# Kernel tuning notes

Hardware: AMD Instinct MI355X
Metric: run time of the kernel (lower is better)

Reference implementation:

```python
import jax, jax.numpy as jnp
import numpy as np

N, E, G = 100000, 1600000, 1024
BN_EPS = 1e-5
NEG_SLOPE = 0.2


def setup_inputs() -> dict:
    key = jax.random.key(0)
    ks = jax.random.split(key, 8)
    x = jax.random.normal(ks[0], (N, 128), dtype=jnp.float32)
    edge_index = jax.random.randint(ks[1], (2, E), 0, N, dtype=jnp.int64)
    batch = jnp.sort(jax.random.randint(ks[2], (N,), 0, G, dtype=jnp.int64))
    Wl = jax.random.normal(ks[3], (3, 128, 128), dtype=jnp.float32) * 0.08
    bl = jnp.zeros((3, 128), dtype=jnp.float32)
    Wr = jax.random.normal(ks[4], (3, 128, 128), dtype=jnp.float32) * 0.08
    bn_gamma = jnp.ones((3, 128), dtype=jnp.float32)
    bn_beta = jnp.zeros((3, 128), dtype=jnp.float32)
    bn2_gamma = jnp.ones((128,), dtype=jnp.float32)
    bn2_beta = jnp.zeros((128,), dtype=jnp.float32)
    fc_W = jax.random.normal(ks[5], (128, 64), dtype=jnp.float32) * 0.08
    fc_b = jnp.zeros((64,), dtype=jnp.float32)
    return {"x": x, "edge_index": edge_index, "batch": batch, "Wl": Wl, "bl": bl,
            "Wr": Wr, "bn_gamma": bn_gamma, "bn_beta": bn_beta,
            "bn2_gamma": bn2_gamma, "bn2_beta": bn2_beta, "fc_W": fc_W, "fc_b": fc_b}


def _batch_norm(h, gamma, beta):
    # training-mode BatchNorm1d: batch statistics, biased variance
    mu = jnp.mean(h, axis=0)
    var = jnp.mean((h - mu) ** 2, axis=0)
    return gamma * (h - mu) * jax.lax.rsqrt(var + BN_EPS) + beta


def reference(x, edge_index, batch, Wl, bl, Wr, bn_gamma, bn_beta,
              bn2_gamma, bn2_beta, fc_W, fc_b):
    src, dst = edge_index[0], edge_index[1]
    # in-degree of each destination node (for mean aggregation)
    deg = jax.ops.segment_sum(jnp.ones((E,), dtype=x.dtype), dst, num_segments=N)
    inv_deg = jnp.where(deg > 0, 1.0 / jnp.maximum(deg, 1.0), 0.0)[:, None]  # [N,1]
    h = x
    for i in range(3):
        # SAGEConv: out = lin_l(mean_{j in N(i)} h_j) + lin_r(h_i)
        agg = jax.ops.segment_sum(h[src], dst, num_segments=N) * inv_deg  # [N,H]
        h = agg @ Wl[i] + bl[i] + h @ Wr[i]
        h = jax.nn.leaky_relu(_batch_norm(h, bn_gamma[i], bn_beta[i]), NEG_SLOPE)
        # dropout omitted (eval-mode / deterministic reference)
    pooled = jax.ops.segment_sum(h, batch, num_segments=G)  # [G,H] global_add_pool
    out = _batch_norm(pooled, bn2_gamma, bn2_beta) @ fc_W + fc_b  # [G,latent]
    return out
```

## Files before the change

kernel.cpp:

```cpp
#include <hip/hip_runtime.h>

#define HD 128
#define NCOPY 32
#define BSH 8
#define BSZ 256
#define EPB 4096

typedef __attribute__((ext_vector_type(8))) short short8;
typedef __attribute__((ext_vector_type(4))) float f32x4;

union ABu { unsigned long long u[2]; short8 s8; };

__device__ inline float bf2f(ushort u) {
    union { unsigned int i; float f; } x; x.i = ((unsigned int)u) << 16; return x.f;
}
__device__ inline float bflo(unsigned int u) {
    union { unsigned int i; float f; } x; x.i = u << 16; return x.f;
}
__device__ inline float bfhi(unsigned int u) {
    union { unsigned int i; float f; } x; x.i = u & 0xffff0000u; return x.f;
}
__device__ inline ushort f2bf(float f) {
    union { float f; unsigned int i; } x; x.f = f;
    unsigned int r = x.i + 0x7FFF + ((x.i >> 16) & 1);
    return (ushort)(r >> 16);
}


__global__ __launch_bounds__(256) void kp_count(const int* __restrict__ dst,
                                                int* __restrict__ bucketCount, int E, int NB) {
    __shared__ int hist[512];
    for (int i = threadIdx.x; i < NB; i += 256) hist[i] = 0;
    __syncthreads();
    int e0 = blockIdx.x * EPB;
#pragma unroll
    for (int j = 0; j < 16; ++j) {
        int e = e0 + j * 256 + threadIdx.x;
        if (e < E) atomicAdd(&hist[dst[e] >> BSH], 1);
    }
    __syncthreads();
    for (int i = threadIdx.x; i < NB; i += 256)
        if (hist[i]) atomicAdd(&bucketCount[i], hist[i]);
}

__global__ void kp_scan(const int* __restrict__ bucketCount, int* __restrict__ bucketBase,
                        int* __restrict__ gCursor, int NB, int E) {
    __shared__ int lds[512];
    int tid = threadIdx.x;
    int v = (tid < NB) ? bucketCount[tid] : 0;
    lds[tid] = v;
    __syncthreads();
    for (int off = 1; off < 512; off <<= 1) {
        int t = 0;
        if (tid >= off) t = lds[tid - off];
        __syncthreads();
        if (tid >= off) lds[tid] += t;
        __syncthreads();
    }
    int excl = lds[tid] - v;
    if (tid < NB) { bucketBase[tid] = excl; gCursor[tid] = excl; }
    if (tid == 0) bucketBase[NB] = E;
}

__global__ __launch_bounds__(256) void kp_part(const int* __restrict__ src,
                                               const int* __restrict__ dst,
                                               int* __restrict__ gCursor,
                                               unsigned int* __restrict__ packed, int E, int NB) {
    __shared__ int hist[512], lbase[512], lcur[512];
    for (int i = threadIdx.x; i < NB; i += 256) hist[i] = 0;
    __syncthreads();
    int e0 = blockIdx.x * EPB;
    int b[16]; unsigned int w[16];
#pragma unroll
    for (int j = 0; j < 16; ++j) {
        int e = e0 + j * 256 + threadIdx.x;
        b[j] = -1;
        if (e < E) {
            int d = dst[e];
            int s = src[e];
            b[j] = d >> BSH;
            w[j] = (unsigned int)s | (((unsigned int)d & (BSZ - 1)) << 17);
            atomicAdd(&hist[b[j]], 1);
        }
    }
    __syncthreads();
    for (int i = threadIdx.x; i < NB; i += 256) {
        int c = hist[i];
        lbase[i] = c ? atomicAdd(&gCursor[i], c) : 0;
        lcur[i] = 0;
    }
    __syncthreads();
#pragma unroll
    for (int j = 0; j < 16; ++j) {
        if (b[j] >= 0) {
            int r = atomicAdd(&lcur[b[j]], 1);
            packed[lbase[b[j]] + r] = w[j];
        }
    }
}

__global__ __launch_bounds__(256) void kp_degfill(const unsigned int* __restrict__ packed,
                                                  const int* __restrict__ bucketBase,
                                                  int* __restrict__ rowptr,
                                                  float* __restrict__ inv,
                                                  int* __restrict__ csr, int N, int E) {
    __shared__ int dcnt[BSZ];
    __shared__ int scn[BSZ];
    __shared__ int rp[BSZ];
    int bkt = blockIdx.x;
    int tid = threadIdx.x;
    int n0 = bkt << BSH;
    dcnt[tid] = 0;
    __syncthreads();
    int beg = bucketBase[bkt], end = bucketBase[bkt + 1];
    for (int e = beg + tid; e < end; e += 256)
        atomicAdd(&dcnt[packed[e] >> 17], 1);
    __syncthreads();
    int v = dcnt[tid];
    scn[tid] = v;
    __syncthreads();
    for (int off = 1; off < 256; off <<= 1) {
        int t = 0;
        if (tid >= off) t = scn[tid - off];
        __syncthreads();
        if (tid >= off) scn[tid] += t;
        __syncthreads();
    }
    int rpv = beg + scn[tid] - v;
    int n = n0 + tid;
    if (n < N) {
        rowptr[n] = rpv;
        inv[n] = (v > 0) ? (1.0f / (float)v) : 0.0f;
    }
    if (bkt == 0 && tid == 0) rowptr[N] = E;
    __syncthreads();
    dcnt[tid] = 0;
    rp[tid] = rpv;
    __syncthreads();
    for (int e = beg + tid; e < end; e += 256) {
        unsigned int wv = packed[e];
        int ld = wv >> 17;
        int p = atomicAdd(&dcnt[ld], 1);
        csr[rp[ld] + p] = (int)(wv & 0x1FFFF);
    }
}

__global__ void k_prep(const float* __restrict__ x, ushort* __restrict__ xb, int total4,
                       const float* __restrict__ Wl, const float* __restrict__ Wr,
                       ushort* __restrict__ WT, int wtTotal) {
    int i = blockIdx.x * blockDim.x + threadIdx.x;
    int stride = gridDim.x * blockDim.x;
    for (int idx = i; idx < total4; idx += stride) {
        float4 v = ((const float4*)x)[idx];
        ushort4 o;
        o.x = f2bf(v.x); o.y = f2bf(v.y); o.z = f2bf(v.z); o.w = f2bf(v.w);
        ((ushort4*)xb)[idx] = o;
    }
    for (int idx = i; idx < wtTotal; idx += stride) {
        int l = idx >> 15;
        int rem = idx & 32767;
        int col = rem >> 8;
        int k = rem & 255;
        float v = (k < 128) ? Wl[l * 16384 + k * 128 + col]
                            : Wr[l * 16384 + (k - 128) * 128 + col];
        WT[idx] = f2bf(v);
    }
}

__global__ __launch_bounds__(256) void k_agg(const ushort* __restrict__ h,
                                             const int* __restrict__ rowptr,
                                             const int* __restrict__ csr,
                                             const float* __restrict__ inv,
                                             ushort* __restrict__ agg, int N) {
    int node = blockIdx.x * 4 + (threadIdx.x >> 6);
    if (node >= N) return;
    int lane = threadIdx.x & 63;
    int g = lane >> 4, ln = lane & 15;
    int beg = rowptr[node], end = rowptr[node + 1];
    float a[8], b[8];
#pragma unroll
    for (int j = 0; j < 8; ++j) { a[j] = 0.f; b[j] = 0.f; }
    for (int e = beg + g; e < end; e += 8) {
        int s0 = csr[e];
        uint4 v0 = *(const uint4*)&h[(size_t)s0 * HD + ln * 8];
        int e1 = e + 4;
        if (e1 < end) {
            int s1 = csr[e1];
            uint4 v1 = *(const uint4*)&h[(size_t)s1 * HD + ln * 8];
            b[0] += bflo(v1.x); b[1] += bfhi(v1.x);
            b[2] += bflo(v1.y); b[3] += bfhi(v1.y);
            b[4] += bflo(v1.z); b[5] += bfhi(v1.z);
            b[6] += bflo(v1.w); b[7] += bfhi(v1.w);
        }
        a[0] += bflo(v0.x); a[1] += bfhi(v0.x);
        a[2] += bflo(v0.y); a[3] += bfhi(v0.y);
        a[4] += bflo(v0.z); a[5] += bfhi(v0.z);
        a[6] += bflo(v0.w); a[7] += bfhi(v0.w);
    }
#pragma unroll
    for (int j = 0; j < 8; ++j) {
        a[j] += b[j];
        a[j] += __shfl_xor(a[j], 16);
        a[j] += __shfl_xor(a[j], 32);
    }
    if (lane < 16) {
        float iv = inv[node];
        ushort o[8];
#pragma unroll
        for (int j = 0; j < 8; ++j) o[j] = f2bf(a[j] * iv);
        *(uint4*)&agg[(size_t)node * HD + ln * 8] = *(uint4*)o;
    }
}

__global__ __launch_bounds__(256) void k_gemm(
        const ushort* __restrict__ X1, const ushort* __restrict__ X2,
        const ushort* __restrict__ WT, const float* __restrict__ bias,
        ushort* __restrict__ out, float* __restrict__ stats, int N) {
    __shared__ ushort As[128 * 72];
    __shared__ ushort Bs[128 * 72];
    int tid = threadIdx.x;
    int lane = tid & 63, wid = tid >> 6;
    int wr = wid >> 1, wc = wid & 1;
    int ln15 = lane & 15, kg = lane >> 4;
    int rbase = blockIdx.x * 128;
    int r0 = tid >> 3, q8 = (tid & 7) * 8;

    f32x4 acc[4][4];
#pragma unroll
    for (int m = 0; m < 4; ++m)
#pragma unroll
        for (int nn = 0; nn < 4; ++nn) acc[m][nn] = (f32x4){0.f, 0.f, 0.f, 0.f};

    uint4 ra[4], rb[4];
    auto loadchunk = [&](int c) {
        const ushort* X = (c < 2) ? X1 : X2;
        int cb = (c & 1) * 64;
#pragma unroll
        for (int p = 0; p < 4; ++p) {
            int r = r0 + p * 32;
            int grow = rbase + r;
            uint4 v = {0u, 0u, 0u, 0u};
            if (grow < N) v = *(const uint4*)&X[(size_t)grow * HD + cb + q8];
            ra[p] = v;
            rb[p] = *(const uint4*)&WT[r * 256 + c * 64 + q8];
        }
    };
    loadchunk(0);

    for (int c = 0; c < 4; ++c) {
#pragma unroll
        for (int p = 0; p < 4; ++p) {
            int r = r0 + p * 32;
            *(uint4*)&As[r * 72 + q8] = ra[p];
            *(uint4*)&Bs[r * 72 + q8] = rb[p];
        }
        __syncthreads();
        if (c < 3) loadchunk(c + 1);
#pragma unroll
        for (int kk = 0; kk < 2; ++kk) {
            short8 af[4], bfr[4];
#pragma unroll
            for (int m = 0; m < 4; ++m) {
                int row = wr * 64 + m * 16 + ln15;
                const ushort* pa = &As[row * 72 + kk * 32 + kg * 4];
                ABu u; u.u[0] = *(const unsigned long long*)pa;
                u.u[1] = *(const unsigned long long*)(pa + 16);
                af[m] = u.s8;
            }
#pragma unroll
            for (int nn = 0; nn < 4; ++nn) {
                int col = wc * 64 + nn * 16 + ln15;
                const ushort* pb = &Bs[col * 72 + kk * 32 + kg * 4];
                ABu u; u.u[0] = *(const unsigned long long*)pb;
                u.u[1] = *(const unsigned long long*)(pb + 16);
                bfr[nn] = u.s8;
            }
#pragma unroll
            for (int m = 0; m < 4; ++m)
#pragma unroll
                for (int nn = 0; nn < 4; ++nn)
                    acc[m][nn] = __builtin_amdgcn_mfma_f32_16x16x32_bf16(af[m], bfr[nn], acc[m][nn], 0, 0, 0);
        }
        __syncthreads();
    }

    float s[4] = {0.f, 0.f, 0.f, 0.f};
    float q[4] = {0.f, 0.f, 0.f, 0.f};
    float bv[4];
#pragma unroll
    for (int nn = 0; nn < 4; ++nn) bv[nn] = bias[wc * 64 + nn * 16 + ln15];
#pragma unroll
    for (int m = 0; m < 4; ++m) {
#pragma unroll
        for (int j = 0; j < 4; ++j) {
            int row = rbase + wr * 64 + m * 16 + kg * 4 + j;
            if (row < N) {
#pragma unroll
                for (int nn = 0; nn < 4; ++nn) {
                    float v = acc[m][nn][j] + bv[nn];
                    out[(size_t)row * HD + wc * 64 + nn * 16 + ln15] = f2bf(v);
                    s[nn] += v; q[nn] += v * v;
                }
            }
        }
    }
#pragma unroll
    for (int nn = 0; nn < 4; ++nn) {
        s[nn] += __shfl_xor(s[nn], 16); s[nn] += __shfl_xor(s[nn], 32);
        q[nn] += __shfl_xor(q[nn], 16); q[nn] += __shfl_xor(q[nn], 32);
    }
    if (lane < 16) {
        int slot = (blockIdx.x & (NCOPY - 1)) * 256;
#pragma unroll
        for (int nn = 0; nn < 4; ++nn) {
            int col = wc * 64 + nn * 16 + lane;
            atomicAdd(&stats[slot + col], s[nn]);
            atomicAdd(&stats[slot + 128 + col], q[nn]);
        }
    }
}

__global__ __launch_bounds__(256) void k_apply(ushort* buf, const float* __restrict__ stats,
                                               const float* __restrict__ gamma,
                                               const float* __restrict__ beta,
                                               float count, int total8) {
    __shared__ float sc[HD], sh[HD];
    int tid = threadIdx.x;
    if (tid < HD) {
        float s = 0.f, q = 0.f;
        for (int i = 0; i < NCOPY; ++i) { s += stats[i * 256 + tid]; q += stats[i * 256 + 128 + tid]; }
        float mean = s / count;
        float var = fmaxf(q / count - mean * mean, 0.f);
        float scale = gamma[tid] * rsqrtf(var + 1e-5f);
        sc[tid] = scale;
        sh[tid] = beta[tid] - mean * scale;
    }
    __syncthreads();
    int i = blockIdx.x * blockDim.x + tid;
    int stride = gridDim.x * blockDim.x;
    for (int idx = i; idx < total8; idx += stride) {
        int cb = (idx * 8) & (HD - 1);
        uint4 v = ((const uint4*)buf)[idx];
        float f[8];
        f[0] = bflo(v.x); f[1] = bfhi(v.x);
        f[2] = bflo(v.y); f[3] = bfhi(v.y);
        f[4] = bflo(v.z); f[5] = bfhi(v.z);
        f[6] = bflo(v.w); f[7] = bfhi(v.w);
        ushort o[8];
#pragma unroll
        for (int j = 0; j < 8; ++j) {
            float y = f[j] * sc[cb + j] + sh[cb + j];
            y = (y > 0.f) ? y : 0.2f * y;
            o[j] = f2bf(y);
        }
        ((uint4*)buf)[idx] = *(uint4*)o;
    }
}

__global__ void k_poolapply(const ushort* __restrict__ h, const float* __restrict__ stats,
                            const float* __restrict__ gamma, const float* __restrict__ beta,
                            float count, const int* __restrict__ batch,
                            float* __restrict__ pooled, int N) {
    int c = threadIdx.x;
    float s = 0.f, q = 0.f;
    for (int i = 0; i < NCOPY; ++i) { s += stats[i * 256 + c]; q += stats[i * 256 + 128 + c]; }
    float mean = s / count;
    float var = fmaxf(q / count - mean * mean, 0.f);
    float sc = gamma[c] * rsqrtf(var + 1e-5f);
    float sh = beta[c] - mean * sc;
    int n0 = blockIdx.x * 16;
    if (n0 >= N) return;
    int nend = min(n0 + 16, N);
    float acc = 0.f;
    int cur = batch[n0];
    for (int n = n0; n < nend; ++n) {
        int b = batch[n];
        if (b != cur) { atomicAdd(&pooled[cur * HD + c], acc); acc = 0.f; cur = b; }
        float y = bf2f(h[(size_t)n * HD + c]) * sc + sh;
        y = (y > 0.f) ? y : 0.2f * y;
        acc += y;
    }
    atomicAdd(&pooled[cur * HD + c], acc);
}

__global__ void k_colstats(const float* __restrict__ X, float* __restrict__ stats, int rows) {
    int c = threadIdx.x;
    float s = 0.f, q = 0.f;
    for (int r = blockIdx.x; r < rows; r += gridDim.x) {
        float v = X[r * HD + c];
        s += v; q += v * v;
    }
    int slot = (blockIdx.x & (NCOPY - 1)) * 256;
    atomicAdd(&stats[slot + c], s);
    atomicAdd(&stats[slot + 128 + c], q);
}

__global__ void k_final(const float* __restrict__ pooled, const float* __restrict__ stats2,
                        const float* __restrict__ bn2g, const float* __restrict__ bn2b,
                        const float* __restrict__ fcW, const float* __restrict__ fcb,
                        float* __restrict__ outp, float countG) {
    __shared__ float Wlds[HD * 64];
    __shared__ float prow[HD];
    int tid = threadIdx.x;
    for (int i = tid; i < HD * 64 / 4; i += 128) ((float4*)Wlds)[i] = ((const float4*)fcW)[i];
    float s = 0.f, q = 0.f;
    for (int i = 0; i < NCOPY; ++i) { s += stats2[i * 256 + tid]; q += stats2[i * 256 + 128 + tid]; }
    float mean = s / countG;
    float var = fmaxf(q / countG - mean * mean, 0.f);
    float scale = bn2g[tid] * rsqrtf(var + 1e-5f);
    float shift = bn2b[tid] - mean * scale;
    int g = blockIdx.x;
    prow[tid] = pooled[g * HD + tid] * scale + shift;
    __syncthreads();
    if (tid < 64) {
        float acc = fcb[tid];
#pragma unroll 8
        for (int c = 0; c < HD; ++c) acc += prow[c] * Wlds[c * 64 + tid];
        outp[g * 64 + tid] = acc;
    }
}

extern "C" void kernel_launch(void* const* d_in, const int* in_sizes, int n_in,
                              void* d_out, int out_size, void* d_ws, size_t ws_size,
                              hipStream_t stream) {
    const float* x     = (const float*)d_in[0];
    const int*   ei    = (const int*)d_in[1];
    const int*   batch = (const int*)d_in[2];
    const float* Wl    = (const float*)d_in[3];
    const float* bl    = (const float*)d_in[4];
    const float* Wr    = (const float*)d_in[5];
    const float* bng   = (const float*)d_in[6];
    const float* bnb   = (const float*)d_in[7];
    const float* bn2g  = (const float*)d_in[8];
    const float* bn2b  = (const float*)d_in[9];
    const float* fcW   = (const float*)d_in[10];
    const float* fcb   = (const float*)d_in[11];

    int N = in_sizes[0] / HD;
    int E = in_sizes[1] / 2;
    int G = out_size / 64;
    const int* src = ei;
    const int* dst = ei + E;

    char* p = (char*)d_ws;
    auto alloc = [&](size_t bytes) -> void* {
        void* r = (void*)p;
        p += (bytes + 255) & ~(size_t)255;
        return r;
    };
    int NB = (N + BSZ - 1) >> BSH;
    int nPB = (E + EPB - 1) / EPB;

    int*    rowptr   = (int*)alloc((size_t)(N + 1) * 4);
    int*    bCount   = (int*)alloc((size_t)NB * 4);
    int*    bBase    = (int*)alloc((size_t)(NB + 1) * 4);
    int*    gCursor  = (int*)alloc((size_t)NB * 4);
    int*    csr      = (int*)alloc((size_t)E * 4);
    float*  inv      = (float*)alloc((size_t)N * 4);
    ushort* WT       = (ushort*)alloc((size_t)3 * 128 * 256 * 2);
    ushort* xb       = (ushort*)alloc((size_t)N * HD * 2);
    ushort* aggb     = (ushort*)alloc((size_t)N * HD * 2);
    ushort* hb1      = (ushort*)alloc((size_t)N * HD * 2);
    ushort* hb2      = (ushort*)alloc((size_t)N * HD * 2);
    float*  statsAll = (float*)alloc((size_t)4 * NCOPY * 256 * 4);
    float*  pooled   = (float*)alloc((size_t)G * HD * 4);

    float* stats0  = statsAll;
    float* stats1  = statsAll + NCOPY * 256;
    float* statsL2 = statsAll + 2 * NCOPY * 256;
    float* stats2  = statsAll + 3 * NCOPY * 256;

    unsigned int* packed = (unsigned int*)aggb;

    float* outp = (float*)d_out;
    int total4 = N * HD / 4;
    int total8 = N * HD / 8;
    int ggrid = (N + 127) / 128;
    int agrid = (N + 3) / 4;
    float fN = (float)N, fG = (float)G;

    hipMemsetAsync(statsAll, 0, (size_t)4 * NCOPY * 256 * 4 + (size_t)G * HD * 4, stream);
    hipMemsetAsync(bCount, 0, (size_t)NB * 4, stream);
    k_prep<<<2048, 256, 0, stream>>>(x, xb, total4, Wl, Wr, WT, 3 * 128 * 256);

    kp_count<<<nPB, 256, 0, stream>>>(dst, bCount, E, NB);
    kp_scan<<<1, 512, 0, stream>>>(bCount, bBase, gCursor, NB, E);
    kp_part<<<nPB, 256, 0, stream>>>(src, dst, gCursor, packed, E, NB);
    kp_degfill<<<NB, 256, 0, stream>>>(packed, bBase, rowptr, inv, csr, N, E);

    k_agg<<<agrid, 256, 0, stream>>>(xb, rowptr, csr, inv, aggb, N);
    k_gemm<<<ggrid, 256, 0, stream>>>(aggb, xb, WT, bl, hb1, stats0, N);
    k_apply<<<2048, 256, 0, stream>>>(hb1, stats0, bng, bnb, fN, total8);

    k_agg<<<agrid, 256, 0, stream>>>(hb1, rowptr, csr, inv, aggb, N);
    k_gemm<<<ggrid, 256, 0, stream>>>(aggb, hb1, WT + 32768, bl + 128, hb2, stats1, N);
    k_apply<<<2048, 256, 0, stream>>>(hb2, stats1, bng + 128, bnb + 128, fN, total8);

    k_agg<<<agrid, 256, 0, stream>>>(hb2, rowptr, csr, inv, aggb, N);
    k_gemm<<<ggrid, 256, 0, stream>>>(aggb, hb2, WT + 65536, bl + 256, hb1, statsL2, N);
    k_poolapply<<<(N + 15) / 16, HD, 0, stream>>>(hb1, statsL2, bng + 256, bnb + 256, fN,
                                                  batch, pooled, N);

    k_colstats<<<64, HD, 0, stream>>>(pooled, stats2, G);
    k_final<<<G, HD, 0, stream>>>(pooled, stats2, bn2g, bn2b, fcW, fcb, outp, fG);
}
```

Measured before the change: 421.3 us.

## Merge preprocessing launches, inline bucket scan, simplify GEMM loads, coarsen pooling

```diff
diff --git a/kernel.cpp b/kernel.cpp
--- a/kernel.cpp
+++ b/kernel.cpp
@@ -26,54 +26,78 @@
     return (ushort)(r >> 16);
 }
 
-
-__global__ __launch_bounds__(256) void kp_count(const int* __restrict__ dst,
-                                                int* __restrict__ bucketCount, int E, int NB) {
+__global__ __launch_bounds__(256) void k_prepcount(
+        const float* __restrict__ x, ushort* __restrict__ xb, int total4,
+        const float* __restrict__ Wl, const float* __restrict__ Wr,
+        ushort* __restrict__ WT, int wtTotal,
+        const int* __restrict__ dst, int* __restrict__ bucketCount, int E, int NB, int nPB) {
     __shared__ int hist[512];
-    for (int i = threadIdx.x; i < NB; i += 256) hist[i] = 0;
-    __syncthreads();
-    int e0 = blockIdx.x * EPB;
-#pragma unroll
-    for (int j = 0; j < 16; ++j) {
-        int e = e0 + j * 256 + threadIdx.x;
-        if (e < E) atomicAdd(&hist[dst[e] >> BSH], 1);
-    }
-    __syncthreads();
-    for (int i = threadIdx.x; i < NB; i += 256)
-        if (hist[i]) atomicAdd(&bucketCount[i], hist[i]);
-}
-
-__global__ void kp_scan(const int* __restrict__ bucketCount, int* __restrict__ bucketBase,
-                        int* __restrict__ gCursor, int NB, int E) {
-    __shared__ int lds[512];
-    int tid = threadIdx.x;
-    int v = (tid < NB) ? bucketCount[tid] : 0;
-    lds[tid] = v;
-    __syncthreads();
-    for (int off = 1; off < 512; off <<= 1) {
-        int t = 0;
-        if (tid >= off) t = lds[tid - off];
-        __syncthreads();
-        if (tid >= off) lds[tid] += t;
-        __syncthreads();
-    }
-    int excl = lds[tid] - v;
-    if (tid < NB) { bucketBase[tid] = excl; gCursor[tid] = excl; }
-    if (tid == 0) bucketBase[NB] = E;
+    if (blockIdx.x < nPB) {
+        for (int i = threadIdx.x; i < NB; i += 256) hist[i] = 0;
+        __syncthreads();
+        int e0 = blockIdx.x * EPB;
+#pragma unroll
+        for (int j = 0; j < 16; ++j) {
+            int e = e0 + j * 256 + threadIdx.x;
+            if (e < E) atomicAdd(&hist[dst[e] >> BSH], 1);
+        }
+        __syncthreads();
+        for (int i = threadIdx.x; i < NB; i += 256)
+            if (hist[i]) atomicAdd(&bucketCount[i], hist[i]);
+    } else {
+        int i = (blockIdx.x - nPB) * 256 + threadIdx.x;
+        int stride = (gridDim.x - nPB) * 256;
+        for (int idx = i; idx < total4; idx += stride) {
+            float4 v = ((const float4*)x)[idx];
+            ushort4 o;
+            o.x = f2bf(v.x); o.y = f2bf(v.y); o.z = f2bf(v.z); o.w = f2bf(v.w);
+            ((ushort4*)xb)[idx] = o;
+        }
+        for (int idx = i; idx < wtTotal; idx += stride) {
+            int l = idx >> 15;
+            int rem = idx & 32767;
+            int col = rem >> 8;
+            int k = rem & 255;
+            float v = (k < 128) ? Wl[l * 16384 + k * 128 + col]
+                                : Wr[l * 16384 + (k - 128) * 128 + col];
+            WT[idx] = f2bf(v);
+        }
+    }
 }
 
 __global__ __launch_bounds__(256) void kp_part(const int* __restrict__ src,
                                                const int* __restrict__ dst,
+                                               const int* __restrict__ bCount,
                                                int* __restrict__ gCursor,
-                                               unsigned int* __restrict__ packed, int E, int NB) {
+                                               unsigned int* __restrict__ packed,
+                                               int E, int NB) {
+    __shared__ int bbase[512];
+    __shared__ int pair[256];
     __shared__ int hist[512], lbase[512], lcur[512];
-    for (int i = threadIdx.x; i < NB; i += 256) hist[i] = 0;
-    __syncthreads();
+    int tid = threadIdx.x;
+    int i0 = 2 * tid, i1 = 2 * tid + 1;
+    int v0 = (i0 < NB) ? bCount[i0] : 0;
+    int v1 = (i1 < NB) ? bCount[i1] : 0;
+    pair[tid] = v0 + v1;
+    __syncthreads();
+    for (int off = 1; off < 256; off <<= 1) {
+        int t = 0;
+        if (tid >= off) t = pair[tid - off];
+        __syncthreads();
+        if (tid >= off) pair[tid] += t;
+        __syncthreads();
+    }
+    int incl = pair[tid];
+    bbase[i0] = incl - v0 - v1;
+    bbase[i1] = incl - v1;
+    for (int i = tid; i < NB; i += 256) hist[i] = 0;
+    __syncthreads();
+
     int e0 = blockIdx.x * EPB;
     int b[16]; unsigned int w[16];
 #pragma unroll
     for (int j = 0; j < 16; ++j) {
-        int e = e0 + j * 256 + threadIdx.x;
+        int e = e0 + j * 256 + tid;
         b[j] = -1;
         if (e < E) {
             int d = dst[e];
@@ -84,9 +108,9 @@
         }
     }
     __syncthreads();
-    for (int i = threadIdx.x; i < NB; i += 256) {
+    for (int i = tid; i < NB; i += 256) {
         int c = hist[i];
-        lbase[i] = c ? atomicAdd(&gCursor[i], c) : 0;
+        lbase[i] = c ? (bbase[i] + atomicAdd(&gCursor[i], c)) : 0;
         lcur[i] = 0;
     }
     __syncthreads();
@@ -100,19 +124,30 @@
 }
 
 __global__ __launch_bounds__(256) void kp_degfill(const unsigned int* __restrict__ packed,
-                                                  const int* __restrict__ bucketBase,
+                                                  const int* __restrict__ bCount,
                                                   int* __restrict__ rowptr,
                                                   float* __restrict__ inv,
-                                                  int* __restrict__ csr, int N, int E) {
+                                                  int* __restrict__ csr, int N, int E, int NB) {
     __shared__ int dcnt[BSZ];
     __shared__ int scn[BSZ];
     __shared__ int rp[BSZ];
+    __shared__ int red[256];
     int bkt = blockIdx.x;
     int tid = threadIdx.x;
     int n0 = bkt << BSH;
+    int partial = 0;
+    for (int i = tid; i < bkt; i += 256) partial += bCount[i];
+    red[tid] = partial;
+    __syncthreads();
+    for (int off = 128; off > 0; off >>= 1) {
+        if (tid < off) red[tid] += red[tid + off];
+        __syncthreads();
+    }
+    int beg = red[0];
+    int end = beg + bCount[bkt];
+    __syncthreads();
     dcnt[tid] = 0;
     __syncthreads();
-    int beg = bucketBase[bkt], end = bucketBase[bkt + 1];
     for (int e = beg + tid; e < end; e += 256)
         atomicAdd(&dcnt[packed[e] >> 17], 1);
     __syncthreads();
@@ -142,28 +177,6 @@
         int ld = wv >> 17;
         int p = atomicAdd(&dcnt[ld], 1);
         csr[rp[ld] + p] = (int)(wv & 0x1FFFF);
-    }
-}
-
-__global__ void k_prep(const float* __restrict__ x, ushort* __restrict__ xb, int total4,
-                       const float* __restrict__ Wl, const float* __restrict__ Wr,
-                       ushort* __restrict__ WT, int wtTotal) {
-    int i = blockIdx.x * blockDim.x + threadIdx.x;
-    int stride = gridDim.x * blockDim.x;
-    for (int idx = i; idx < total4; idx += stride) {
-        float4 v = ((const float4*)x)[idx];
-        ushort4 o;
-        o.x = f2bf(v.x); o.y = f2bf(v.y); o.z = f2bf(v.z); o.w = f2bf(v.w);
-        ((ushort4*)xb)[idx] = o;
-    }
-    for (int idx = i; idx < wtTotal; idx += stride) {
-        int l = idx >> 15;
-        int rem = idx & 32767;
-        int col = rem >> 8;
-        int k = rem & 255;
-        float v = (k < 128) ? Wl[l * 16384 + k * 128 + col]
-                            : Wr[l * 16384 + (k - 128) * 128 + col];
-        WT[idx] = f2bf(v);
     }
 }
 
@@ -223,7 +236,6 @@
     int wr = wid >> 1, wc = wid & 1;
     int ln15 = lane & 15, kg = lane >> 4;
     int rbase = blockIdx.x * 128;
-    int r0 = tid >> 3, q8 = (tid & 7) * 8;
 
     f32x4 acc[4][4];
 #pragma unroll
@@ -231,31 +243,25 @@
 #pragma unroll
         for (int nn = 0; nn < 4; ++nn) acc[m][nn] = (f32x4){0.f, 0.f, 0.f, 0.f};
 
-    uint4 ra[4], rb[4];
-    auto loadchunk = [&](int c) {
+    for (int c = 0; c < 4; ++c) {
         const ushort* X = (c < 2) ? X1 : X2;
         int cb = (c & 1) * 64;
 #pragma unroll
         for (int p = 0; p < 4; ++p) {
-            int r = r0 + p * 32;
+            int g = tid + p * 256;
+            int r = g >> 3, q = g & 7;
             int grow = rbase + r;
             uint4 v = {0u, 0u, 0u, 0u};
-            if (grow < N) v = *(const uint4*)&X[(size_t)grow * HD + cb + q8];
-            ra[p] = v;
-            rb[p] = *(const uint4*)&WT[r * 256 + c * 64 + q8];
-        }
-    };
-    loadchunk(0);
-
-    for (int c = 0; c < 4; ++c) {
+            if (grow < N) v = *(const uint4*)&X[(size_t)grow * HD + cb + q * 8];
+            *(uint4*)&As[r * 72 + q * 8] = v;
+        }
 #pragma unroll
         for (int p = 0; p < 4; ++p) {
-            int r = r0 + p * 32;
-            *(uint4*)&As[r * 72 + q8] = ra[p];
-            *(uint4*)&Bs[r * 72 + q8] = rb[p];
-        }
-        __syncthreads();
-        if (c < 3) loadchunk(c + 1);
+            int g = tid + p * 256;
+            int col = g >> 3, q = g & 7;
+            *(uint4*)&Bs[col * 72 + q * 8] = *(const uint4*)&WT[col * 256 + c * 64 + q * 8];
+        }
+        __syncthreads();
 #pragma unroll
         for (int kk = 0; kk < 2; ++kk) {
             short8 af[4], bfr[4];
@@ -368,9 +374,9 @@
     float var = fmaxf(q / count - mean * mean, 0.f);
     float sc = gamma[c] * rsqrtf(var + 1e-5f);
     float sh = beta[c] - mean * sc;
-    int n0 = blockIdx.x * 16;
+    int n0 = blockIdx.x * 64;
     if (n0 >= N) return;
-    int nend = min(n0 + 16, N);
+    int nend = min(n0 + 64, N);
     float acc = 0.f;
     int cur = batch[n0];
     for (int n = n0; n < nend; ++n) {
@@ -452,9 +458,6 @@
     int nPB = (E + EPB - 1) / EPB;
 
     int*    rowptr   = (int*)alloc((size_t)(N + 1) * 4);
-    int*    bCount   = (int*)alloc((size_t)NB * 4);
-    int*    bBase    = (int*)alloc((size_t)(NB + 1) * 4);
-    int*    gCursor  = (int*)alloc((size_t)NB * 4);
     int*    csr      = (int*)alloc((size_t)E * 4);
     float*  inv      = (float*)alloc((size_t)N * 4);
     ushort* WT       = (ushort*)alloc((size_t)3 * 128 * 256 * 2);
@@ -462,8 +465,12 @@
     ushort* aggb     = (ushort*)alloc((size_t)N * HD * 2);
     ushort* hb1      = (ushort*)alloc((size_t)N * HD * 2);
     ushort* hb2      = (ushort*)alloc((size_t)N * HD * 2);
+    char*   zbase    = (char*)alloc(0);
     float*  statsAll = (float*)alloc((size_t)4 * NCOPY * 256 * 4);
     float*  pooled   = (float*)alloc((size_t)G * HD * 4);
+    int*    bCount   = (int*)alloc((size_t)NB * 4);
+    int*    gCursor  = (int*)alloc((size_t)NB * 4);
+    size_t  zbytes   = (size_t)((char*)p - zbase);
 
     float* stats0  = statsAll;
     float* stats1  = statsAll + NCOPY * 256;
@@ -479,14 +486,11 @@
     int agrid = (N + 3) / 4;
     float fN = (float)N, fG = (float)G;
 
-    hipMemsetAsync(statsAll, 0, (size_t)4 * NCOPY * 256 * 4 + (size_t)G * HD * 4, stream);
-    hipMemsetAsync(bCount, 0, (size_t)NB * 4, stream);
-    k_prep<<<2048, 256, 0, stream>>>(x, xb, total4, Wl, Wr, WT, 3 * 128 * 256);
-
-    kp_count<<<nPB, 256, 0, stream>>>(dst, bCount, E, NB);
-    kp_scan<<<1, 512, 0, stream>>>(bCount, bBase, gCursor, NB, E);
-    kp_part<<<nPB, 256, 0, stream>>>(src, dst, gCursor, packed, E, NB);
-    kp_degfill<<<NB, 256, 0, stream>>>(packed, bBase, rowptr, inv, csr, N, E);
+    hipMemsetAsync(zbase, 0, zbytes, stream);
+    k_prepcount<<<nPB + 1024, 256, 0, stream>>>(x, xb, total4, Wl, Wr, WT, 3 * 128 * 256,
+                                                dst, bCount, E, NB, nPB);
+    kp_part<<<nPB, 256, 0, stream>>>(src, dst, bCount, gCursor, packed, E, NB);
+    kp_degfill<<<NB, 256, 0, stream>>>(packed, bCount, rowptr, inv, csr, N, E, NB);
 
     k_agg<<<agrid, 256, 0, stream>>>(xb, rowptr, csr, inv, aggb, N);
     k_gemm<<<ggrid, 256, 0, stream>>>(aggb, xb, WT, bl, hb1, stats0, N);
@@ -498,7 +502,7 @@
 
     k_agg<<<agrid, 256, 0, stream>>>(hb2, rowptr, csr, inv, aggb, N);
     k_gemm<<<ggrid, 256, 0, stream>>>(aggb, hb2, WT + 65536, bl + 256, hb1, statsL2, N);
-    k_poolapply<<<(N + 15) / 16, HD, 0, stream>>>(hb1, statsL2, bng + 256, bnb + 256, fN,
+    k_poolapply<<<(N + 63) / 64, HD, 0, stream>>>(hb1, statsL2, bng + 256, bnb + 256, fN,
                                                   batch, pooled, N);
 
     k_colstats<<<64, HD, 0, stream>>>(pooled, stats2, G);
```

Result: faster. 397.1 us (-5.7%).
